# Optimization experiments

Hardware: AMD Instinct MI355X
Metric: run time of the kernel (lower is better)

Reference implementation:

```python
import jax, jax.numpy as jnp
import numpy as np

D_MODEL = 1024
N_HEADS = 16
HEAD_DIM = D_MODEL // N_HEADS
BLOCK_SIZE = 2048
B, T = 4, 2048


def setup_inputs() -> dict:
    key = jax.random.key(0)
    ks = jax.random.split(key, 5)
    s = 0.02
    x = jax.random.normal(ks[0], (B, T, D_MODEL), dtype=jnp.float32)
    W_qkv = jax.random.normal(ks[1], (D_MODEL, 3 * D_MODEL), dtype=jnp.float32) * s
    b_qkv = jnp.zeros((3 * D_MODEL,), dtype=jnp.float32)
    W_proj = jax.random.normal(ks[2], (D_MODEL, D_MODEL), dtype=jnp.float32) * s
    b_proj = jnp.zeros((D_MODEL,), dtype=jnp.float32)
    return {"x": x, "W_qkv": W_qkv, "b_qkv": b_qkv, "W_proj": W_proj, "b_proj": b_proj}


def reference(x, W_qkv, b_qkv, W_proj, b_proj):
    Bsz, Tlen, C = x.shape
    qkv = x @ W_qkv + b_qkv                      # [B,T,3C]
    q, k, v = jnp.split(qkv, 3, axis=2)
    # [B,T,C] -> [B,H,T,hd]
    def heads(t):
        return t.reshape(Bsz, Tlen, N_HEADS, HEAD_DIM).transpose(0, 2, 1, 3)
    q, k, v = heads(q), heads(k), heads(v)
    scale = 1.0 / jnp.sqrt(jnp.asarray(HEAD_DIM, dtype=x.dtype))
    att = jnp.einsum('bhqd,bhkd->bhqk', q, k) * scale   # [B,H,T,T]
    causal = jnp.tril(jnp.ones((Tlen, Tlen), dtype=bool))
    att = jnp.where(causal, att, jnp.asarray(-jnp.inf, dtype=att.dtype))
    att = jax.nn.softmax(att, axis=-1)
    y = jnp.einsum('bhqk,bhkd->bhqd', att, v)            # [B,H,T,hd]
    y = y.transpose(0, 2, 1, 3).reshape(Bsz, Tlen, C)
    return y @ W_proj + b_proj
```

## Files before the change

### kernel.cpp

```cpp
#include <hip/hip_runtime.h>
#include <hip/hip_bf16.h>

#define D_MODEL 1024
#define N_HEADS 16
#define HEAD_DIM 64
#define SEQ_T 2048
#define BATCH 4

#define SL2E 0.18033688011f

typedef short s8v  __attribute__((ext_vector_type(8)));
typedef float f32x4 __attribute__((ext_vector_type(4)));
typedef unsigned long long ull;

static __device__ __forceinline__ unsigned short f2bf(float f) {
  union { float f; unsigned int u; } v; v.f = f;
  unsigned int u = v.u;
  return (unsigned short)((u + 0x7FFF + ((u >> 16) & 1)) >> 16);
}

static __device__ __forceinline__ unsigned int cvtpk_bf16(float lo, float hi) {
  unsigned int r;
  asm("v_cvt_pk_bf16_f32 %0, %1, %2" : "=v"(r) : "v"(lo), "v"(hi));
  return r;
}

#if __has_builtin(__builtin_amdgcn_exp2f)
#define EXP2(x) __builtin_amdgcn_exp2f(x)
#else
#define EXP2(x) exp2f(x)
#endif

static __device__ __forceinline__ void glds16(const void* g, void* l) {
  __builtin_amdgcn_global_load_lds(
      (const __attribute__((address_space(1))) void*)g,
      (__attribute__((address_space(3))) void*)l, 16, 0, 0);
}

template<int MODE>
__global__ __launch_bounds__(256) void gemm_bt_kernel(
    const unsigned short* __restrict__ A, const unsigned short* __restrict__ Bt,
    const float* __restrict__ bias, float* __restrict__ Cout,
    unsigned short* __restrict__ qkb, unsigned short* __restrict__ vT,
    int M, int N, int K)
{
  __shared__ unsigned short Al[128 * 64];
  __shared__ unsigned short Bl[128 * 64];

  const int tid  = threadIdx.x;
  const int lane = tid & 63;
  const int wave = tid >> 6;
  const int col  = lane & 15;
  const int quad = lane >> 4;
  const int wm   = (wave & 1) * 64;
  const int wn   = (wave >> 1) * 64;
  const int bm0  = blockIdx.y * 128;
  const int bn0  = blockIdx.x * 128;
  const int cx   = col & 7;

  f32x4 acc[4][4];
  #pragma unroll
  for (int t = 0; t < 4; ++t)
    #pragma unroll
    for (int u = 0; u < 4; ++u) acc[t][u] = (f32x4)0.f;

  for (int k0 = 0; k0 < K; k0 += 64) {
    __syncthreads();
    #pragma unroll
    for (int i = 0; i < 4; ++i) {
      int idx = i * 256 + tid;
      int row = idx >> 3;
      int gc  = (idx & 7) ^ (row & 7);
      glds16(A  + (size_t)(bm0 + row) * K + k0 + gc * 8, &Al[idx * 8]);
      glds16(Bt + (size_t)(bn0 + row) * K + k0 + gc * 8, &Bl[idx * 8]);
    }
    __syncthreads();

    #pragma unroll
    for (int s = 0; s < 2; ++s) {
      s8v af[4], bf[4];
      #pragma unroll
      for (int t = 0; t < 4; ++t) {
        int ar = wm + t * 16 + col;
        af[t] = *(const s8v*)&Al[ar * 64 + (((s * 4 + quad) ^ cx) * 8)];
        int br = wn + t * 16 + col;
        bf[t] = *(const s8v*)&Bl[br * 64 + (((s * 4 + quad) ^ cx) * 8)];
      }
      #pragma unroll
      for (int t = 0; t < 4; ++t)
        #pragma unroll
        for (int u = 0; u < 4; ++u)
          acc[t][u] = __builtin_amdgcn_mfma_f32_16x16x32_bf16(
              af[t], bf[u], acc[t][u], 0, 0, 0);
    }
  }

  float bv[4];
  #pragma unroll
  for (int u = 0; u < 4; ++u) bv[u] = bias[bn0 + wn + u * 16 + col];

  if (MODE == 1 && bn0 >= 2048) {
    #pragma unroll
    for (int t = 0; t < 4; ++t) {
      int m_base = bm0 + wm + t * 16 + quad * 4;
      #pragma unroll
      for (int u = 0; u < 4; ++u) {
        int hd = (bn0 + wn + u * 16 + col) - 2048;
        size_t bh = (size_t)(bm0 >> 11) * 16 + (hd >> 6);
        ull pk = (ull)f2bf(acc[t][u][0] + bv[u])
               | ((ull)f2bf(acc[t][u][1] + bv[u]) << 16)
               | ((ull)f2bf(acc[t][u][2] + bv[u]) << 32)
               | ((ull)f2bf(acc[t][u][3] + bv[u]) << 48);
        *(ull*)(vT + (bh * 64 + (hd & 63)) * 2048 + (m_base & 2047)) = pk;
      }
    }
  } else {
    const float sc = (MODE == 1 && (bn0 + wn) < 1024) ? SL2E : 1.0f;
    #pragma unroll
    for (int t = 0; t < 4; ++t) {
      #pragma unroll
      for (int r = 0; r < 4; ++r) {
        size_t m = bm0 + wm + t * 16 + quad * 4 + r;
        #pragma unroll
        for (int u = 0; u < 4; ++u) {
          int n = bn0 + wn + u * 16 + col;
          float v = acc[t][u][r] + bv[u];
          if (MODE == 0) Cout[m * N + n] = v;
          else           qkb[m * 2048 + n] = f2bf(v * sc);
        }
      }
    }
  }
}

static __device__ __forceinline__ void transpose_tile(
    const float* __restrict__ W, unsigned short* __restrict__ Wt,
    int K, int N, int n0, int k0)
{
  __shared__ float tile[32][33];
  const int tx = threadIdx.x & 31, ty = threadIdx.x >> 5;
  #pragma unroll
  for (int i = 0; i < 4; ++i)
    tile[ty + i * 8][tx] = W[(size_t)(k0 + ty + i * 8) * N + n0 + tx];
  __syncthreads();
  #pragma unroll
  for (int i = 0; i < 4; ++i)
    Wt[(size_t)(n0 + ty + i * 8) * K + k0 + tx] = f2bf(tile[tx][ty + i * 8]);
}

__global__ __launch_bounds__(256) void prep_kernel(
    const float* __restrict__ x, const float* __restrict__ W_qkv,
    const float* __restrict__ W_proj, ushort4* __restrict__ xb,
    unsigned short* __restrict__ wqt, unsigned short* __restrict__ wpt)
{
  const int bid = blockIdx.x;
  if (bid < 8192) {
    int i = bid * 256 + threadIdx.x;
    float4 v = ((const float4*)x)[i];
    ushort4 o;
    o.x = f2bf(v.x); o.y = f2bf(v.y); o.z = f2bf(v.z); o.w = f2bf(v.w);
    xb[i] = o;
  } else if (bid < 8192 + 3072) {
    int b2 = bid - 8192;
    transpose_tile(W_qkv, wqt, 1024, 3072, (b2 % 96) * 32, (b2 / 96) * 32);
  } else {
    int b3 = bid - 11264;
    transpose_tile(W_proj, wpt, 1024, 1024, (b3 % 32) * 32, (b3 / 32) * 32);
  }
}

#define LPAD 72

__global__ __launch_bounds__(256, 3) void attn_mfma_kernel(
    const unsigned short* __restrict__ qk, const unsigned short* __restrict__ vT,
    unsigned short* __restrict__ y)
{
  __shared__ unsigned short Ks[2][64 * 64];
  __shared__ unsigned short Vs[2][64 * 64];
  __shared__ unsigned short Ps[128][LPAD];

  const int tid  = threadIdx.x;
  const int wave = tid >> 6;
  const int lane = tid & 63;
  const int col  = lane & 15;
  const int quad = lane >> 4;
  const int cx   = col & 7;

  const int bh = blockIdx.x;
  const int b = bh >> 4, h = bh & 15;
  const int qblk = 15 - (int)blockIdx.y;
  const int q0 = qblk * 128;
  const int nk = 2 * qblk + 2;
  const int C2 = 2048;

  const unsigned short* qbase = qk + (size_t)b * SEQ_T * C2 + h * 64;
  const unsigned short* kbase = qbase + 1024;
  const unsigned short* vbase = vT + (size_t)bh * 64 * 2048;

  s8v qf[2][2];
  #pragma unroll
  for (int s = 0; s < 2; ++s)
    #pragma unroll
    for (int c = 0; c < 2; ++c)
      qf[s][c] = *(const s8v*)(qbase +
          (size_t)(q0 + s * 64 + wave * 16 + col) * C2 + c * 32 + quad * 8);

  f32x4 acc[2][4];
  #pragma unroll
  for (int s = 0; s < 2; ++s)
    #pragma unroll
    for (int t = 0; t < 4; ++t) acc[s][t] = (f32x4)0.f;
  float lsum[2] = {0.f, 0.f};

  auto stage = [&](int kt, int bi) {
    const int k0 = kt * 64;
    #pragma unroll
    for (int i = 0; i < 2; ++i) {
      int cid = (i * 4 + wave) * 64 + lane;
      int row = cid >> 3;
      int gc  = (cid & 7) ^ (row & 7);
      glds16(kbase + (size_t)(k0 + row) * C2 + gc * 8, &Ks[bi][cid * 8]);
      glds16(vbase + (size_t)row * 2048 + k0 + gc * 8, &Vs[bi][cid * 8]);
    }
  };

  auto tile_body = [&](int kt, int bi) {
    const int k0 = kt * 64;

    s8v kf[4][2];
    #pragma unroll
    for (int t = 0; t < 4; ++t)
      #pragma unroll
      for (int c = 0; c < 2; ++c)
        kf[t][c] = *(const s8v*)&Ks[bi][(t * 16 + col) * 64 + (((c * 4 + quad) ^ cx) * 8)];

    #pragma unroll
    for (int s = 0; s < 2; ++s) {
      const int qs = q0 + s * 64 + wave * 16;
      if (k0 > qs + 15) continue;

      f32x4 st[4];
      #pragma unroll
      for (int t = 0; t < 4; ++t) st[t] = (f32x4)0.f;
      #pragma unroll
      for (int t = 0; t < 4; ++t)
        #pragma unroll
        for (int c = 0; c < 2; ++c)
          st[t] = __builtin_amdgcn_mfma_f32_16x16x32_bf16(kf[t][c], qf[s][c], st[t], 0, 0, 0);

      const bool diag = (k0 + 63 > qs);
      if (!diag) {
        #pragma unroll
        for (int t = 0; t < 4; ++t) {
          float e0 = EXP2(st[t][0]);
          float e1 = EXP2(st[t][1]);
          float e2 = EXP2(st[t][2]);
          float e3 = EXP2(st[t][3]);
          lsum[s] += (e0 + e1) + (e2 + e3);
          uint2 pk;
          pk.x = cvtpk_bf16(e0, e1);
          pk.y = cvtpk_bf16(e2, e3);
          *(uint2*)&Ps[s * 64 + wave * 16 + col][t * 16 + quad * 4] = pk;
        }
      } else {
        const int qg = qs + col;
        #pragma unroll
        for (int t = 0; t < 4; ++t) {
          uint2 pk;
          if (k0 + t * 16 > qs + 15) {
            pk.x = 0u; pk.y = 0u;
          } else {
            float e[4];
            #pragma unroll
            for (int r = 0; r < 4; ++r) {
              float v = EXP2(st[t][r]);
              if (k0 + t * 16 + quad * 4 + r > qg) v = 0.f;
              e[r] = v;
            }
            lsum[s] += (e[0] + e[1]) + (e[2] + e[3]);
            pk.x = cvtpk_bf16(e[0], e[1]);
            pk.y = cvtpk_bf16(e[2], e[3]);
          }
          *(uint2*)&Ps[s * 64 + wave * 16 + col][t * 16 + quad * 4] = pk;
        }
      }
    }

    s8v vf[4][2];
    #pragma unroll
    for (int t = 0; t < 4; ++t)
      #pragma unroll
      for (int c = 0; c < 2; ++c)
        vf[t][c] = *(const s8v*)&Vs[bi][(t * 16 + col) * 64 + (((c * 4 + quad) ^ cx) * 8)];
    #pragma unroll
    for (int s = 0; s < 2; ++s) {
      const int qs = q0 + s * 64 + wave * 16;
      if (k0 > qs + 15) continue;
      s8v pf[2];
      #pragma unroll
      for (int c = 0; c < 2; ++c)
        pf[c] = *(const s8v*)&Ps[s * 64 + wave * 16 + col][c * 32 + quad * 8];
      #pragma unroll
      for (int t = 0; t < 4; ++t)
        #pragma unroll
        for (int c = 0; c < 2; ++c)
          acc[s][t] = __builtin_amdgcn_mfma_f32_16x16x32_bf16(pf[c], vf[t][c], acc[s][t], 0, 0, 0);
    }
  };

  stage(0, 0);
  for (int kt = 0; kt < nk; kt += 2) {
    __syncthreads();
    if (kt + 1 < nk) stage(kt + 1, 1);
    tile_body(kt, 0);
    if (kt + 1 < nk) {
      __syncthreads();
      if (kt + 2 < nk) stage(kt + 2, 0);
      tile_body(kt + 1, 1);
    }
  }

  #pragma unroll
  for (int s = 0; s < 2; ++s) {
    float v = lsum[s];
    v += __shfl_xor(v, 16);
    v += __shfl_xor(v, 32);
    #pragma unroll
    for (int r = 0; r < 4; ++r) {
      float inv = 1.0f / __shfl(v, quad * 4 + r);
      int q = q0 + s * 64 + wave * 16 + quad * 4 + r;
      unsigned short* yrow = y + (size_t)(b * SEQ_T + q) * D_MODEL + h * 64;
      #pragma unroll
      for (int t = 0; t < 4; ++t)
        yrow[t * 16 + col] = f2bf(acc[s][t][r] * inv);
    }
  }
}

extern "C" void kernel_launch(void* const* d_in, const int* in_sizes, int n_in,
                              void* d_out, int out_size, void* d_ws, size_t ws_size,
                              hipStream_t stream) {
  const float* x      = (const float*)d_in[0];
  const float* W_qkv  = (const float*)d_in[1];
  const float* b_qkv  = (const float*)d_in[2];
  const float* W_proj = (const float*)d_in[3];
  const float* b_proj = (const float*)d_in[4];
  float* out = (float*)d_out;

  const int M  = BATCH * SEQ_T;
  const int C  = D_MODEL;
  const int C3 = 3 * D_MODEL;

  unsigned short* xb  = (unsigned short*)d_ws;
  unsigned short* wqt = xb  + (size_t)M * C;
  unsigned short* wpt = wqt + (size_t)C3 * C;
  unsigned short* qkb = wpt + (size_t)C * C;
  unsigned short* vTb = qkb + (size_t)M * 2 * C;
  unsigned short* yb  = vTb + (size_t)64 * 64 * SEQ_T;

  dim3 blk(256);

  prep_kernel<<<dim3(8192 + 3072 + 1024), blk, 0, stream>>>(
      x, W_qkv, W_proj, (ushort4*)xb, wqt, wpt);

  gemm_bt_kernel<1><<<dim3(C3 / 128, M / 128), blk, 0, stream>>>(
      xb, wqt, b_qkv, nullptr, qkb, vTb, M, C3, C);

  attn_mfma_kernel<<<dim3(BATCH * N_HEADS, SEQ_T / 128), blk, 0, stream>>>(
      qkb, vTb, yb);

  gemm_bt_kernel<0><<<dim3(C / 128, M / 128), blk, 0, stream>>>(
      yb, wpt, b_proj, out, nullptr, nullptr, M, C, C);
}
```

Baseline: 239.6 us.

## Double-buffer GEMM tiles with 256x128 blocks and interleaved async loads

```diff
diff --git a/kernel.cpp b/kernel.cpp
--- a/kernel.cpp
+++ b/kernel.cpp
@@ -37,26 +37,31 @@
       (__attribute__((address_space(3))) void*)l, 16, 0, 0);
 }
 
+#define BARRIER() do { asm volatile("" ::: "memory"); \
+                       __builtin_amdgcn_s_barrier();  \
+                       asm volatile("" ::: "memory"); } while (0)
+
 template<int MODE>
-__global__ __launch_bounds__(256) void gemm_bt_kernel(
+__global__ __launch_bounds__(512, 2) void gemm_bt_kernel(
     const unsigned short* __restrict__ A, const unsigned short* __restrict__ Bt,
     const float* __restrict__ bias, float* __restrict__ Cout,
     unsigned short* __restrict__ qkb, unsigned short* __restrict__ vT,
     int M, int N, int K)
 {
-  __shared__ unsigned short Al[128 * 64];
-  __shared__ unsigned short Bl[128 * 64];
+  __shared__ unsigned short As[2][256 * 64];
+  __shared__ unsigned short Bs[2][128 * 64];
 
   const int tid  = threadIdx.x;
   const int lane = tid & 63;
-  const int wave = tid >> 6;
+  const int wid  = tid >> 6;
   const int col  = lane & 15;
   const int quad = lane >> 4;
-  const int wm   = (wave & 1) * 64;
-  const int wn   = (wave >> 1) * 64;
-  const int bm0  = blockIdx.y * 128;
+  const int cx   = col & 7;
+  const int wr   = wid >> 1;
+  const int wc   = wid & 1;
+  const int bm0  = blockIdx.y * 256;
   const int bn0  = blockIdx.x * 128;
-  const int cx   = col & 7;
+  const int NT   = K >> 6;
 
   f32x4 acc[4][4];
   #pragma unroll
@@ -64,67 +69,138 @@
     #pragma unroll
     for (int u = 0; u < 4; ++u) acc[t][u] = (f32x4)0.f;
 
-  for (int k0 = 0; k0 < K; k0 += 64) {
-    __syncthreads();
-    #pragma unroll
-    for (int i = 0; i < 4; ++i) {
-      int idx = i * 256 + tid;
+  auto stageA = [&](int t, int bi, int h) {
+    const int k0 = t * 64;
+    #pragma unroll
+    for (int l = 0; l < 2; ++l) {
+      int idx = l * 512 + tid;
+      int row = h * 128 + (idx >> 3);
+      int gc  = (idx & 7) ^ (row & 7);
+      glds16(A + (size_t)(bm0 + row) * K + k0 + gc * 8,
+             &As[bi][(h * 1024 + idx) * 8]);
+    }
+  };
+  auto stageB = [&](int t, int bi) {
+    const int k0 = t * 64;
+    #pragma unroll
+    for (int l = 0; l < 2; ++l) {
+      int idx = l * 512 + tid;
       int row = idx >> 3;
       int gc  = (idx & 7) ^ (row & 7);
-      glds16(A  + (size_t)(bm0 + row) * K + k0 + gc * 8, &Al[idx * 8]);
-      glds16(Bt + (size_t)(bn0 + row) * K + k0 + gc * 8, &Bl[idx * 8]);
-    }
-    __syncthreads();
-
-    #pragma unroll
-    for (int s = 0; s < 2; ++s) {
-      s8v af[4], bf[4];
-      #pragma unroll
-      for (int t = 0; t < 4; ++t) {
-        int ar = wm + t * 16 + col;
-        af[t] = *(const s8v*)&Al[ar * 64 + (((s * 4 + quad) ^ cx) * 8)];
-        int br = wn + t * 16 + col;
-        bf[t] = *(const s8v*)&Bl[br * 64 + (((s * 4 + quad) ^ cx) * 8)];
-      }
-      #pragma unroll
-      for (int t = 0; t < 4; ++t)
-        #pragma unroll
-        for (int u = 0; u < 4; ++u)
-          acc[t][u] = __builtin_amdgcn_mfma_f32_16x16x32_bf16(
-              af[t], bf[u], acc[t][u], 0, 0, 0);
-    }
+      glds16(Bt + (size_t)(bn0 + row) * K + k0 + gc * 8, &Bs[bi][idx * 8]);
+    }
+  };
+
+  auto body = [&](int t, int bi) {
+    s8v af[4][2], bf[4][2];
+    if (t + 1 < NT) stageB(t + 1, bi ^ 1);
+    #pragma unroll
+    for (int tm = 0; tm < 4; ++tm)
+      #pragma unroll
+      for (int kh = 0; kh < 2; ++kh)
+        af[tm][kh] = *(const s8v*)&As[bi][(wr * 64 + tm * 16 + col) * 64 +
+                                          (((kh * 4 + quad) ^ cx) * 8)];
+    #pragma unroll
+    for (int u = 0; u < 4; ++u)
+      #pragma unroll
+      for (int kh = 0; kh < 2; ++kh)
+        bf[u][kh] = *(const s8v*)&Bs[bi][(wc * 64 + u * 16 + col) * 64 +
+                                         (((kh * 4 + quad) ^ cx) * 8)];
+    __builtin_amdgcn_s_setprio(1);
+    #pragma unroll
+    for (int tm = 0; tm < 2; ++tm)
+      #pragma unroll
+      for (int u = 0; u < 2; ++u)
+        #pragma unroll
+        for (int kh = 0; kh < 2; ++kh)
+          acc[tm][u] = __builtin_amdgcn_mfma_f32_16x16x32_bf16(
+              af[tm][kh], bf[u][kh], acc[tm][u], 0, 0, 0);
+    __builtin_amdgcn_s_setprio(0);
+    asm volatile("s_waitcnt lgkmcnt(0)" ::: "memory");
+    __builtin_amdgcn_sched_barrier(0);
+    BARRIER();
+
+    if (t + 2 < NT) stageA(t + 2, bi, 0);
+    __builtin_amdgcn_s_setprio(1);
+    #pragma unroll
+    for (int tm = 0; tm < 2; ++tm)
+      #pragma unroll
+      for (int u = 2; u < 4; ++u)
+        #pragma unroll
+        for (int kh = 0; kh < 2; ++kh)
+          acc[tm][u] = __builtin_amdgcn_mfma_f32_16x16x32_bf16(
+              af[tm][kh], bf[u][kh], acc[tm][u], 0, 0, 0);
+    __builtin_amdgcn_s_setprio(0);
+    BARRIER();
+
+    if (t + 2 < NT) stageA(t + 2, bi, 1);
+    __builtin_amdgcn_s_setprio(1);
+    #pragma unroll
+    for (int tm = 2; tm < 4; ++tm)
+      #pragma unroll
+      for (int u = 2; u < 4; ++u)
+        #pragma unroll
+        for (int kh = 0; kh < 2; ++kh)
+          acc[tm][u] = __builtin_amdgcn_mfma_f32_16x16x32_bf16(
+              af[tm][kh], bf[u][kh], acc[tm][u], 0, 0, 0);
+    __builtin_amdgcn_s_setprio(0);
+    BARRIER();
+
+    __builtin_amdgcn_s_setprio(1);
+    #pragma unroll
+    for (int tm = 2; tm < 4; ++tm)
+      #pragma unroll
+      for (int u = 0; u < 2; ++u)
+        #pragma unroll
+        for (int kh = 0; kh < 2; ++kh)
+          acc[tm][u] = __builtin_amdgcn_mfma_f32_16x16x32_bf16(
+              af[tm][kh], bf[u][kh], acc[tm][u], 0, 0, 0);
+    __builtin_amdgcn_s_setprio(0);
+    if (t + 2 < NT) asm volatile("s_waitcnt vmcnt(4)" ::: "memory");
+    else            asm volatile("s_waitcnt vmcnt(0)" ::: "memory");
+    BARRIER();
+  };
+
+  stageA(0, 0, 0); stageA(0, 0, 1); stageB(0, 0);
+  stageA(1, 1, 0); stageA(1, 1, 1);
+  asm volatile("s_waitcnt vmcnt(4)" ::: "memory");
+  BARRIER();
+
+  for (int t = 0; t < NT; t += 2) {
+    body(t, 0);
+    body(t + 1, 1);
   }
 
   float bv[4];
   #pragma unroll
-  for (int u = 0; u < 4; ++u) bv[u] = bias[bn0 + wn + u * 16 + col];
+  for (int u = 0; u < 4; ++u) bv[u] = bias[bn0 + wc * 64 + u * 16 + col];
 
   if (MODE == 1 && bn0 >= 2048) {
     #pragma unroll
-    for (int t = 0; t < 4; ++t) {
-      int m_base = bm0 + wm + t * 16 + quad * 4;
+    for (int tm = 0; tm < 4; ++tm) {
+      int m_base = bm0 + wr * 64 + tm * 16 + quad * 4;
       #pragma unroll
       for (int u = 0; u < 4; ++u) {
-        int hd = (bn0 + wn + u * 16 + col) - 2048;
+        int hd = (bn0 + wc * 64 + u * 16 + col) - 2048;
         size_t bh = (size_t)(bm0 >> 11) * 16 + (hd >> 6);
-        ull pk = (ull)f2bf(acc[t][u][0] + bv[u])
-               | ((ull)f2bf(acc[t][u][1] + bv[u]) << 16)
-               | ((ull)f2bf(acc[t][u][2] + bv[u]) << 32)
-               | ((ull)f2bf(acc[t][u][3] + bv[u]) << 48);
+        ull pk = (ull)f2bf(acc[tm][u][0] + bv[u])
+               | ((ull)f2bf(acc[tm][u][1] + bv[u]) << 16)
+               | ((ull)f2bf(acc[tm][u][2] + bv[u]) << 32)
+               | ((ull)f2bf(acc[tm][u][3] + bv[u]) << 48);
         *(ull*)(vT + (bh * 64 + (hd & 63)) * 2048 + (m_base & 2047)) = pk;
       }
     }
   } else {
-    const float sc = (MODE == 1 && (bn0 + wn) < 1024) ? SL2E : 1.0f;
-    #pragma unroll
-    for (int t = 0; t < 4; ++t) {
+    const float sc = (MODE == 1 && bn0 < 1024) ? SL2E : 1.0f;
+    #pragma unroll
+    for (int tm = 0; tm < 4; ++tm) {
       #pragma unroll
       for (int r = 0; r < 4; ++r) {
-        size_t m = bm0 + wm + t * 16 + quad * 4 + r;
+        size_t m = bm0 + wr * 64 + tm * 16 + quad * 4 + r;
         #pragma unroll
         for (int u = 0; u < 4; ++u) {
-          int n = bn0 + wn + u * 16 + col;
-          float v = acc[t][u][r] + bv[u];
+          int n = bn0 + wc * 64 + u * 16 + col;
+          float v = acc[tm][u][r] + bv[u];
           if (MODE == 0) Cout[m * N + n] = v;
           else           qkb[m * 2048 + n] = f2bf(v * sc);
         }
@@ -358,17 +434,15 @@
   unsigned short* vTb = qkb + (size_t)M * 2 * C;
   unsigned short* yb  = vTb + (size_t)64 * 64 * SEQ_T;
 
-  dim3 blk(256);
-
-  prep_kernel<<<dim3(8192 + 3072 + 1024), blk, 0, stream>>>(
+  prep_kernel<<<dim3(8192 + 3072 + 1024), dim3(256), 0, stream>>>(
       x, W_qkv, W_proj, (ushort4*)xb, wqt, wpt);
 
-  gemm_bt_kernel<1><<<dim3(C3 / 128, M / 128), blk, 0, stream>>>(
+  gemm_bt_kernel<1><<<dim3(C3 / 128, M / 256), dim3(512), 0, stream>>>(
       xb, wqt, b_qkv, nullptr, qkb, vTb, M, C3, C);
 
-  attn_mfma_kernel<<<dim3(BATCH * N_HEADS, SEQ_T / 128), blk, 0, stream>>>(
+  attn_mfma_kernel<<<dim3(BATCH * N_HEADS, SEQ_T / 128), dim3(256), 0, stream>>>(
       qkb, vTb, yb);
 
-  gemm_bt_kernel<0><<<dim3(C / 128, M / 128), blk, 0, stream>>>(
+  gemm_bt_kernel<0><<<dim3(C / 128, M / 256), dim3(512), 0, stream>>>(
       yb, wpt, b_proj, out, nullptr, nullptr, M, C, C);
 }
```

Result: no change. 242.4 us (+1.2%).
